# Performance work log

Hardware: AMD Instinct MI355X
Metric: run time of the kernel (lower is better)

Reference implementation:

```python
import jax, jax.numpy as jnp
import numpy as np
from jax import lax

B, S_IN, T_OUT, H, V = 128, 1024, 128, 512, 32


def gru_cell(x, h, Wih, Whh, bih, bhh):
    # PyTorch GRU cell math: gates ordered (r, z, n)
    gi = x @ Wih.T + bih            # (B, 3H)
    gh = h @ Whh.T + bhh            # (B, 3H)
    ir, iz, inn = jnp.split(gi, 3, axis=-1)
    hr, hz, hn = jnp.split(gh, 3, axis=-1)
    r = jax.nn.sigmoid(ir + hr)
    z = jax.nn.sigmoid(iz + hz)
    n = jnp.tanh(inn + r * hn)
    return (1.0 - z) * n + z * h


def setup_inputs() -> dict:
    key = jax.random.key(0)
    ks = jax.random.split(key, 16)
    s = 0.05
    p = lambda k, shape: (jax.random.normal(k, shape, jnp.float32) * s)
    z = lambda n: jnp.zeros((n,), jnp.float32)
    return {
        "x": jax.random.normal(ks[0], (B, S_IN, 2), jnp.float32),
        "embedding": p(ks[1], (V, H)),
        "enc_Wih0": p(ks[2], (3 * H, 2)), "enc_Whh0": p(ks[3], (3 * H, H)),
        "enc_bih0": z(3 * H), "enc_bhh0": z(3 * H),
        "enc_Wih1": p(ks[4], (3 * H, H)), "enc_Whh1": p(ks[5], (3 * H, H)),
        "enc_bih1": z(3 * H), "enc_bhh1": z(3 * H),
        "dec_Wih0": p(ks[6], (3 * H, H)), "dec_Whh0": p(ks[7], (3 * H, H)),
        "dec_bih0": z(3 * H), "dec_bhh0": z(3 * H),
        "dec_Wih1": p(ks[8], (3 * H, H)), "dec_Whh1": p(ks[9], (3 * H, H)),
        "dec_bih1": z(3 * H), "dec_bhh1": z(3 * H),
        "Wq": p(ks[10], (H, H)), "bq": z(H),
        "Wc": p(ks[11], (V, 2 * H)), "bc": z(V),
    }


def reference(x, embedding,
              enc_Wih0, enc_Whh0, enc_bih0, enc_bhh0,
              enc_Wih1, enc_Whh1, enc_bih1, enc_bhh1,
              dec_Wih0, dec_Whh0, dec_bih0, dec_bhh0,
              dec_Wih1, dec_Whh1, dec_bih1, dec_bhh1,
              Wq, bq, Wc, bc):
    b = x.shape[0]
    h_init = jnp.zeros((b, H), x.dtype)

    def run_layer(xs, Wih, Whh, bih, bhh):
        def step(h, xt):
            h2 = gru_cell(xt, h, Wih, Whh, bih, bhh)
            return h2, h2
        return lax.scan(step, h_init, xs)

    # ----- encoder: 2-layer GRU over time -----
    xs = jnp.swapaxes(x, 0, 1)                       # (S, B, 2)
    hT0, ys0 = run_layer(xs, enc_Wih0, enc_Whh0, enc_bih0, enc_bhh0)
    hT1, ys1 = run_layer(ys0, enc_Wih1, enc_Whh1, enc_bih1, enc_bhh1)
    out_enc = jnp.swapaxes(ys1, 0, 1)                # (B, S, H)

    # ----- greedy decoder with Bahdanau-style dot attention -----
    tok0 = jnp.zeros((b,), jnp.int32)                # start token = 0

    def dec_step(carry, _):
        h0, h1, tok = carry
        emb = embedding[tok]                         # (B, H)
        h0n = gru_cell(emb, h0, dec_Wih0, dec_Whh0, dec_bih0, dec_bhh0)
        h1n = gru_cell(h0n, h1, dec_Wih1, dec_Whh1, dec_bih1, dec_bhh1)
        q = h1n @ Wq.T + bq                          # (B, H)
        att = jnp.einsum('bh,bsh->bs', q, out_enc)   # (B, S)
        w = jax.nn.softmax(att, axis=-1)
        ctx = jnp.einsum('bs,bsh->bh', w, out_enc)   # (B, H)
        logits = jnp.concatenate([h1n, ctx], axis=-1) @ Wc.T + bc  # (B, V)
        tok2 = jnp.argmax(logits, axis=-1).astype(jnp.int32)
        return (h0n, h1n, tok2), (logits, w)

    (h0f, h1f, _), (logits_seq, w_seq) = lax.scan(
        dec_step, (hT0, hT1, tok0), None, length=T_OUT)

    vec_out = jnp.swapaxes(logits_seq, 0, 1)         # (B, T_out, V)
    attn_ws = jnp.transpose(w_seq, (1, 2, 0))        # (B, S, T_out)
    hidden = jnp.stack([h0f, h1f], axis=0)           # (n_layers, B, H)
    return vec_out, hidden, attn_ws
```

## Files before the change

### kernel.cpp

```cpp
#include <hip/hip_runtime.h>
#include <hip/hip_fp16.h>
#include <math.h>

#define HH 512
#define BB 128
#define SS 1024
#define TT 128
#define VV 32
#define GG 1536

__device__ __forceinline__ float sigm(float v){ return 1.f/(1.f+expf(-v)); }

struct F8 { float v[8]; };

__device__ __forceinline__ F8 load8(const float* p){
  F8 r;
  float4 a = *reinterpret_cast<const float4*>(p);
  float4 b = *reinterpret_cast<const float4*>(p+4);
  r.v[0]=a.x; r.v[1]=a.y; r.v[2]=a.z; r.v[3]=a.w;
  r.v[4]=b.x; r.v[5]=b.y; r.v[6]=b.z; r.v[7]=b.w;
  return r;
}
__device__ __forceinline__ F8 load8(const __half* p){
  F8 r;
  union { float4 f4; __half2 h2[4]; } u;
  u.f4 = *reinterpret_cast<const float4*>(p);
  #pragma unroll
  for (int i=0;i<4;i++){ float2 f = __half22float2(u.h2[i]); r.v[2*i]=f.x; r.v[2*i+1]=f.y; }
  return r;
}
__device__ __forceinline__ void store_enc(float* p, float v){ *p = v; }
__device__ __forceinline__ void store_enc(__half* p, float v){ *p = __float2half(v); }

__global__ void transpose_k(const float* __restrict__ src, float* __restrict__ dst,
                            int R, int C){
  __shared__ float tile[32][33];
  int c0 = blockIdx.x*32, r0 = blockIdx.y*32;
  int tx = threadIdx.x & 31, ty = threadIdx.x >> 5;
  for (int i = ty; i < 32; i += 8){
    int r = r0 + i, c = c0 + tx;
    tile[i][tx] = (r < R && c < C) ? src[(size_t)r*C + c] : 0.f;
  }
  __syncthreads();
  for (int i = ty; i < 32; i += 8){
    int c = c0 + i, r = r0 + tx;
    if (c < C && r < R) dst[(size_t)c*R + r] = tile[tx][i];
  }
}

template<typename ET>
__global__ __launch_bounds__(192) void enc_step(
    int p,
    const float* __restrict__ x,
    const float* __restrict__ Wih0,
    const float* __restrict__ bih0, const float* __restrict__ bhh0,
    const float* __restrict__ bih1, const float* __restrict__ bhh1,
    const float* __restrict__ Whh0T, const float* __restrict__ Wih1T,
    const float* __restrict__ Whh1T,
    float* __restrict__ gh_all,
    float* __restrict__ h0buf,
    float* __restrict__ h1buf,
    ET* __restrict__ out_enc)
{
  const int bid = blockIdx.x;
  const int xcd = bid & 7, j = bid >> 3;
  const int rc  = xcd*3 + (j % 3);
  const int bch = j / 3;
  const int m   = rc >> 3;
  const int pb  = p & 1;
  if (m == 0 && p >= SS) return;
  if (m >= 1 && p < 1) return;
  const int b0 = bch*8;
  const int tid = threadIdx.x;

  if (m <= 1) {
    float* h0w = h0buf + (size_t)pb*BB*HH;
    for (int idx = tid; idx < 8*HH; idx += 192) {
      int bl = idx >> 9, e = idx & (HH-1);
      int b = b0 + bl;
      float hv;
      if (p == 0) hv = 0.f;
      else {
        int t0 = p - 1;
        float x0v = x[((size_t)b*SS + t0)*2 + 0];
        float x1v = x[((size_t)b*SS + t0)*2 + 1];
        const float* ghp = gh_all + ((size_t)(1-pb)*3 + 0)*BB*GG + (size_t)b*GG;
        float gir = fmaf(x0v, Wih0[e*2],          fmaf(x1v, Wih0[e*2+1],          bih0[e]));
        float giz = fmaf(x0v, Wih0[(HH+e)*2],     fmaf(x1v, Wih0[(HH+e)*2+1],     bih0[HH+e]));
        float gin = fmaf(x0v, Wih0[(2*HH+e)*2],   fmaf(x1v, Wih0[(2*HH+e)*2+1],   bih0[2*HH+e]));
        float ghr = ghp[e]      + bhh0[e];
        float ghz = ghp[HH+e]   + bhh0[HH+e];
        float ghn = ghp[2*HH+e] + bhh0[2*HH+e];
        float hp = (p == 1) ? 0.f : h0buf[(size_t)(1-pb)*BB*HH + (size_t)b*HH + e];
        float r = sigm(gir + ghr);
        float z = sigm(giz + ghz);
        float n = tanhf(fmaf(r, ghn, gin));
        hv = (1.f - z)*n + z*hp;
      }
      h0w[(size_t)b*HH + e] = hv;
    }
  } else {
    float* h1w = h1buf + (size_t)pb*BB*HH;
    for (int idx = tid; idx < 8*HH; idx += 192) {
      int bl = idx >> 9, e = idx & (HH-1);
      int b = b0 + bl;
      float hv;
      if (p <= 1) hv = 0.f;
      else {
        const float* gip = gh_all + ((size_t)(1-pb)*3 + 1)*BB*GG + (size_t)b*GG;
        const float* ghp = gh_all + ((size_t)(1-pb)*3 + 2)*BB*GG + (size_t)b*GG;
        float gir = gip[e]      + bih1[e];
        float giz = gip[HH+e]   + bih1[HH+e];
        float gin = gip[2*HH+e] + bih1[2*HH+e];
        float ghr = ghp[e]      + bhh1[e];
        float ghz = ghp[HH+e]   + bhh1[HH+e];
        float ghn = ghp[2*HH+e] + bhh1[2*HH+e];
        float hp = (p == 2) ? 0.f : h1buf[(size_t)(1-pb)*BB*HH + (size_t)b*HH + e];
        float r = sigm(gir + ghr);
        float z = sigm(giz + ghz);
        float n = tanhf(fmaf(r, ghn, gin));
        hv = (1.f - z)*n + z*hp;
      }
      h1w[(size_t)b*HH + e] = hv;
      if (p >= 2) store_enc(out_enc + ((size_t)b*SS + (p-2))*HH + e, hv);
    }
  }
  __syncthreads();

  const float* WT   = (m == 0) ? Whh0T : (m == 1) ? Wih1T : Whh1T;
  const float* hsrc = (m == 2) ? (h1buf + (size_t)pb*BB*HH) : (h0buf + (size_t)pb*BB*HH);
  const int wv = tid >> 6, lane = tid & 63;
  const int row = (rc & 7)*192 + wv*64 + lane;
  const float* wcol = WT + row;
  float acc[8] = {0,0,0,0,0,0,0,0};
  for (int k = 0; k < HH; k += 4) {
    float w0 = wcol[(size_t)(k+0)*GG];
    float w1 = wcol[(size_t)(k+1)*GG];
    float w2 = wcol[(size_t)(k+2)*GG];
    float w3 = wcol[(size_t)(k+3)*GG];
    #pragma unroll
    for (int i = 0; i < 8; i++) {
      const float4 h4 = *reinterpret_cast<const float4*>(hsrc + (size_t)(b0+i)*HH + k);
      acc[i] = fmaf(w3, h4.w, fmaf(w2, h4.z, fmaf(w1, h4.y, fmaf(w0, h4.x, acc[i]))));
    }
  }
  float* dst = gh_all + ((size_t)pb*3 + m)*BB*GG;
  #pragma unroll
  for (int i = 0; i < 8; i++) dst[(size_t)(b0+i)*GG + row] = acc[i];
}

template<typename ET>
__global__ void enc_bridge(
    const float* __restrict__ gh_all, const float* __restrict__ h1buf,
    const float* __restrict__ bih1, const float* __restrict__ bhh1,
    float* __restrict__ h1init, ET* __restrict__ out_enc)
{
  int idx = blockIdx.x*256 + threadIdx.x;
  int b = idx >> 9, e = idx & (HH-1);
  const float* gip = gh_all + (size_t)1*BB*GG + (size_t)b*GG;
  const float* ghp = gh_all + (size_t)2*BB*GG + (size_t)b*GG;
  float gir = gip[e]      + bih1[e];
  float giz = gip[HH+e]   + bih1[HH+e];
  float gin = gip[2*HH+e] + bih1[2*HH+e];
  float ghr = ghp[e]      + bhh1[e];
  float ghz = ghp[HH+e]   + bhh1[HH+e];
  float ghn = ghp[2*HH+e] + bhh1[2*HH+e];
  float hp = h1buf[(size_t)b*HH + e];
  float r = sigm(gir + ghr);
  float z = sigm(giz + ghz);
  float n = tanhf(fmaf(r, ghn, gin));
  float hv = (1.f - z)*n + z*hp;
  h1init[(size_t)b*HH + e] = hv;
  store_enc(out_enc + ((size_t)b*SS + (SS-1))*HH + e, hv);
}

__global__ __launch_bounds__(192) void dec_step1(
    int t,
    const float* __restrict__ embedding,
    const int* __restrict__ tok,
    const float* __restrict__ bih0d, const float* __restrict__ bhh0d,
    const float* __restrict__ Wih0T, const float* __restrict__ Whh0T,
    const float* __restrict__ h0init,
    float* __restrict__ dgh0,
    float* __restrict__ h0d)
{
  const int bid = blockIdx.x;
  const int xcd = bid & 7, j = bid >> 3;
  const int rc  = xcd*2 + (j & 1);
  const int bch = j >> 1;
  const int m   = rc >> 3;
  const int db  = t & 1;
  const int b0 = bch*8;
  const int tid = threadIdx.x;

  if (m == 1) {
    float* hw = h0d + (size_t)db*BB*HH;
    for (int idx = tid; idx < 8*HH; idx += 192) {
      int bl = idx >> 9, e = idx & (HH-1);
      int b = b0 + bl;
      float hv;
      if (t == 0) hv = h0init[(size_t)b*HH + e];
      else {
        const float* gip = dgh0 + ((size_t)(1-db)*2 + 0)*BB*GG + (size_t)b*GG;
        const float* ghp = dgh0 + ((size_t)(1-db)*2 + 1)*BB*GG + (size_t)b*GG;
        float gir = gip[e]      + bih0d[e];
        float giz = gip[HH+e]   + bih0d[HH+e];
        float gin = gip[2*HH+e] + bih0d[2*HH+e];
        float ghr = ghp[e]      + bhh0d[e];
        float ghz = ghp[HH+e]   + bhh0d[HH+e];
        float ghn = ghp[2*HH+e] + bhh0d[2*HH+e];
        float hp = (t == 1) ? h0init[(size_t)b*HH + e]
                            : h0d[(size_t)(1-db)*BB*HH + (size_t)b*HH + e];
        float r = sigm(gir + ghr);
        float z = sigm(giz + ghz);
        float n = tanhf(fmaf(r, ghn, gin));
        hv = (1.f - z)*n + z*hp;
      }
      hw[(size_t)b*HH + e] = hv;
    }
  }
  __syncthreads();

  const float* WT = (m == 0) ? Wih0T : Whh0T;
  const int wv = tid >> 6, lane = tid & 63;
  const int row = (rc & 7)*192 + wv*64 + lane;
  const float* wcol = WT + row;
  const float* hp8[8];
  #pragma unroll
  for (int i = 0; i < 8; i++)
    hp8[i] = (m == 0) ? (embedding + (size_t)tok[b0+i]*HH)
                      : (h0d + (size_t)db*BB*HH + (size_t)(b0+i)*HH);
  float acc[8] = {0,0,0,0,0,0,0,0};
  for (int k = 0; k < HH; k += 4) {
    float w0 = wcol[(size_t)(k+0)*GG];
    float w1 = wcol[(size_t)(k+1)*GG];
    float w2 = wcol[(size_t)(k+2)*GG];
    float w3 = wcol[(size_t)(k+3)*GG];
    #pragma unroll
    for (int i = 0; i < 8; i++) {
      const float4 h4 = *reinterpret_cast<const float4*>(hp8[i] + k);
      acc[i] = fmaf(w3, h4.w, fmaf(w2, h4.z, fmaf(w1, h4.y, fmaf(w0, h4.x, acc[i]))));
    }
  }
  float* dst = dgh0 + ((size_t)db*2 + m)*BB*GG;
  #pragma unroll
  for (int i = 0; i < 8; i++) dst[(size_t)(b0+i)*GG + row] = acc[i];
}

__global__ __launch_bounds__(192) void dec_step2(
    int t,
    const float* __restrict__ bih0d, const float* __restrict__ bhh0d,
    const float* __restrict__ bih1d, const float* __restrict__ bhh1d,
    const float* __restrict__ Wih1T, const float* __restrict__ Whh1T,
    const float* __restrict__ h1init,
    const float* __restrict__ dgh0,
    const float* __restrict__ h0d,
    float* __restrict__ dgh1,
    float* __restrict__ h1d,
    float* __restrict__ h0n)
{
  const int bid = blockIdx.x;
  const int xcd = bid & 7, j = bid >> 3;
  const int rc  = xcd*2 + (j & 1);
  const int bch = j >> 1;
  const int m   = rc >> 3;
  const int db  = t & 1;
  const int b0 = bch*8;
  const int tid = threadIdx.x;

  if (m == 0) {
    for (int idx = tid; idx < 8*HH; idx += 192) {
      int bl = idx >> 9, e = idx & (HH-1);
      int b = b0 + bl;
      const float* gip = dgh0 + ((size_t)db*2 + 0)*BB*GG + (size_t)b*GG;
      const float* ghp = dgh0 + ((size_t)db*2 + 1)*BB*GG + (size_t)b*GG;
      float gir = gip[e]      + bih0d[e];
      float giz = gip[HH+e]   + bih0d[HH+e];
      float gin = gip[2*HH+e] + bih0d[2*HH+e];
      float ghr = ghp[e]      + bhh0d[e];
      float ghz = ghp[HH+e]   + bhh0d[HH+e];
      float ghn = ghp[2*HH+e] + bhh0d[2*HH+e];
      float hp = h0d[(size_t)db*BB*HH + (size_t)b*HH + e];
      float r = sigm(gir + ghr);
      float z = sigm(giz + ghz);
      float n = tanhf(fmaf(r, ghn, gin));
      h0n[(size_t)b*HH + e] = (1.f - z)*n + z*hp;
    }
  } else {
    float* hw = h1d + (size_t)db*BB*HH;
    for (int idx = tid; idx < 8*HH; idx += 192) {
      int bl = idx >> 9, e = idx & (HH-1);
      int b = b0 + bl;
      float hv;
      if (t == 0) hv = h1init[(size_t)b*HH + e];
      else {
        const float* gip = dgh1 + ((size_t)(1-db)*2 + 0)*BB*GG + (size_t)b*GG;
        const float* ghp = dgh1 + ((size_t)(1-db)*2 + 1)*BB*GG + (size_t)b*GG;
        float gir = gip[e]      + bih1d[e];
        float giz = gip[HH+e]   + bih1d[HH+e];
        float gin = gip[2*HH+e] + bih1d[2*HH+e];
        float ghr = ghp[e]      + bhh1d[e];
        float ghz = ghp[HH+e]   + bhh1d[HH+e];
        float ghn = ghp[2*HH+e] + bhh1d[2*HH+e];
        float hp = (t == 1) ? h1init[(size_t)b*HH + e]
                            : h1d[(size_t)(1-db)*BB*HH + (size_t)b*HH + e];
        float r = sigm(gir + ghr);
        float z = sigm(giz + ghz);
        float n = tanhf(fmaf(r, ghn, gin));
        hv = (1.f - z)*n + z*hp;
      }
      hw[(size_t)b*HH + e] = hv;
    }
  }
  __syncthreads();

  const float* WT = (m == 0) ? Wih1T : Whh1T;
  const float* hsrc = (m == 0) ? h0n : (h1d + (size_t)db*BB*HH);
  const int wv = tid >> 6, lane = tid & 63;
  const int row = (rc & 7)*192 + wv*64 + lane;
  const float* wcol = WT + row;
  float acc[8] = {0,0,0,0,0,0,0,0};
  for (int k = 0; k < HH; k += 4) {
    float w0 = wcol[(size_t)(k+0)*GG];
    float w1 = wcol[(size_t)(k+1)*GG];
    float w2 = wcol[(size_t)(k+2)*GG];
    float w3 = wcol[(size_t)(k+3)*GG];
    #pragma unroll
    for (int i = 0; i < 8; i++) {
      const float4 h4 = *reinterpret_cast<const float4*>(hsrc + (size_t)(b0+i)*HH + k);
      acc[i] = fmaf(w3, h4.w, fmaf(w2, h4.z, fmaf(w1, h4.y, fmaf(w0, h4.x, acc[i]))));
    }
  }
  float* dst = dgh1 + ((size_t)db*2 + m)*BB*GG;
  #pragma unroll
  for (int i = 0; i < 8; i++) dst[(size_t)(b0+i)*GG + row] = acc[i];
}

__global__ __launch_bounds__(256) void dec_step3(
    int t,
    const float* __restrict__ bih1d, const float* __restrict__ bhh1d,
    const float* __restrict__ WqT, const float* __restrict__ bq,
    const float* __restrict__ dgh1, const float* __restrict__ h1d,
    float* __restrict__ h1n, float* __restrict__ qbuf)
{
  const int rc = blockIdx.x & 1, bch = blockIdx.x >> 1;
  const int db = t & 1, b0 = bch*8, tid = threadIdx.x;
  for (int idx = tid; idx < 8*HH; idx += 256) {
    int bl = idx >> 9, e = idx & (HH-1);
    int b = b0 + bl;
    const float* gip = dgh1 + ((size_t)db*2 + 0)*BB*GG + (size_t)b*GG;
    const float* ghp = dgh1 + ((size_t)db*2 + 1)*BB*GG + (size_t)b*GG;
    float gir = gip[e]      + bih1d[e];
    float giz = gip[HH+e]   + bih1d[HH+e];
    float gin = gip[2*HH+e] + bih1d[2*HH+e];
    float ghr = ghp[e]      + bhh1d[e];
    float ghz = ghp[HH+e]   + bhh1d[HH+e];
    float ghn = ghp[2*HH+e] + bhh1d[2*HH+e];
    float hp = h1d[(size_t)db*BB*HH + (size_t)b*HH + e];
    float r = sigm(gir + ghr);
    float z = sigm(giz + ghz);
    float n = tanhf(fmaf(r, ghn, gin));
    h1n[(size_t)b*HH + e] = (1.f - z)*n + z*hp;
  }
  __syncthreads();
  const int wv = tid >> 6, lane = tid & 63;
  const int row = rc*256 + wv*64 + lane;
  const float* wcol = WqT + row;
  float acc[8] = {0,0,0,0,0,0,0,0};
  for (int k = 0; k < HH; k += 4) {
    float w0 = wcol[(size_t)(k+0)*HH];
    float w1 = wcol[(size_t)(k+1)*HH];
    float w2 = wcol[(size_t)(k+2)*HH];
    float w3 = wcol[(size_t)(k+3)*HH];
    #pragma unroll
    for (int i = 0; i < 8; i++) {
      const float4 h4 = *reinterpret_cast<const float4*>(h1n + (size_t)(b0+i)*HH + k);
      acc[i] = fmaf(w3, h4.w, fmaf(w2, h4.z, fmaf(w1, h4.y, fmaf(w0, h4.x, acc[i]))));
    }
  }
  #pragma unroll
  for (int i = 0; i < 8; i++) qbuf[(size_t)(b0+i)*HH + row] = acc[i] + bq[row];
}

template<typename ET>
__global__ __launch_bounds__(256) void dec_attn(
    const float* __restrict__ qbuf, const ET* __restrict__ out_enc,
    float* __restrict__ att, float* __restrict__ pm, float* __restrict__ pl,
    float* __restrict__ pctx)
{
  const int b = blockIdx.x >> 3, sc = blockIdx.x & 7;
  const int tid = threadIdx.x, wv = tid >> 6, lane = tid & 63;
  const F8 q = load8(qbuf + (size_t)b*HH + lane*8);
  const ET* encb = out_enc + (size_t)b*SS*HH;
  float mrun = -1e30f, lrun = 0.f;
  float c[8] = {0,0,0,0,0,0,0,0};
  float attkeep = 0.f;
  const int sbase = sc*128 + wv*32;
  for (int ii = 0; ii < 32; ii++) {
    const F8 e = load8(encb + (size_t)(sbase + ii)*HH + lane*8);
    float d = 0.f;
    #pragma unroll
    for (int j = 0; j < 8; j++) d = fmaf(q.v[j], e.v[j], d);
    #pragma unroll
    for (int off = 32; off >= 1; off >>= 1) d += __shfl_xor(d, off, 64);
    if (lane == ii) attkeep = d;
    float mnew = fmaxf(mrun, d);
    float scal = expf(mrun - mnew);
    float pv = expf(d - mnew);
    lrun = fmaf(lrun, scal, pv);
    #pragma unroll
    for (int j = 0; j < 8; j++) c[j] = fmaf(c[j], scal, pv*e.v[j]);
    mrun = mnew;
  }
  if (lane < 32) att[(size_t)b*SS + sbase + lane] = attkeep;
  __shared__ float lm[4], ll[4];
  __shared__ float lctx[4][HH];
  if (lane == 0) { lm[wv] = mrun; ll[wv] = lrun; }
  #pragma unroll
  for (int j = 0; j < 8; j++) lctx[wv][lane*8+j] = c[j];
  __syncthreads();
  float mb = fmaxf(fmaxf(lm[0],lm[1]), fmaxf(lm[2],lm[3]));
  float e0w = expf(lm[0]-mb), e1w = expf(lm[1]-mb), e2w = expf(lm[2]-mb), e3w = expf(lm[3]-mb);
  if (tid == 0) {
    pm[b*8+sc] = mb;
    pl[b*8+sc] = e0w*ll[0] + e1w*ll[1] + e2w*ll[2] + e3w*ll[3];
  }
  for (int k2 = tid; k2 < HH; k2 += 256) {
    float s = e0w*lctx[0][k2] + e1w*lctx[1][k2] + e2w*lctx[2][k2] + e3w*lctx[3][k2];
    pctx[((size_t)b*8 + sc)*HH + k2] = s;
  }
}

__global__ __launch_bounds__(256) void dec_final(
    int t,
    const float* __restrict__ pm, const float* __restrict__ pl,
    const float* __restrict__ pctx, const float* __restrict__ att,
    const float* __restrict__ h1n,
    const float* __restrict__ WcT, const float* __restrict__ bc,
    float* __restrict__ out_vec, float* __restrict__ out_attn,
    int* __restrict__ tok)
{
  const int b = blockIdx.x, tid = threadIdx.x;
  __shared__ float s_hc[2*HH];
  __shared__ float s_red[8][33];
  float pmv[8], plv[8];
  #pragma unroll
  for (int c = 0; c < 8; c++){ pmv[c] = pm[b*8+c]; plv[c] = pl[b*8+c]; }
  float mg = pmv[0];
  #pragma unroll
  for (int c = 1; c < 8; c++) mg = fmaxf(mg, pmv[c]);
  float epm[8]; float lg = 0.f;
  #pragma unroll
  for (int c = 0; c < 8; c++){ epm[c] = expf(pmv[c]-mg); lg += epm[c]*plv[c]; }
  float inv_lg = 1.f/lg;
  for (int k = tid; k < HH; k += 256) {
    float s = 0.f;
    #pragma unroll
    for (int c = 0; c < 8; c++) s += epm[c]*pctx[((size_t)b*8+c)*HH + k];
    s_hc[HH + k] = s * inv_lg;
    s_hc[k] = h1n[(size_t)b*HH + k];
  }
  __syncthreads();
  for (int s = tid; s < SS; s += 256)
    out_attn[((size_t)b*SS + s)*TT + t] = expf(att[(size_t)b*SS + s] - mg) * inv_lg;
  const int v = tid & 31, part = tid >> 5;
  float pacc = 0.f;
  for (int k = part*128; k < part*128 + 128; k++)
    pacc = fmaf(s_hc[k], WcT[(size_t)k*VV + v], pacc);
  s_red[part][v] = pacc;
  __syncthreads();
  if (tid < 32) {
    float lv = bc[tid];
    #pragma unroll
    for (int c = 0; c < 8; c++) lv += s_red[c][tid];
    out_vec[((size_t)b*TT + t)*VV + tid] = lv;
    float bv = lv; int bi = tid;
    #pragma unroll
    for (int off = 16; off >= 1; off >>= 1) {
      float ov = __shfl_xor(bv, off, 64);
      int   oi = __shfl_xor(bi, off, 64);
      if (ov > bv || (ov == bv && oi < bi)) { bv = ov; bi = oi; }
    }
    if (tid == 0) tok[b] = bi;
  }
}

struct Bufs {
  const float *x, *emb;
  const float *eWih0, *ebih0, *ebhh0, *ebih1, *ebhh1;
  const float *dbih0, *dbhh0, *dbih1, *dbhh1, *bq, *bc;
  float *gh_all, *dgh0, *dgh1;
  float *h0buf, *h1buf, *h0d, *h1d, *h0n, *h1n, *h1init, *qbuf;
  float *att, *pmb, *plb, *pctx;
  int   *tok;
  float *Whh0T, *Wih1T, *Whh1T, *dWih0T, *dWhh0T, *dWih1T, *dWhh1T, *WqT, *WcT;
  float *out_vec, *out_hid, *out_attn;
};

template<typename ET>
static void run_pipeline(const Bufs& B, ET* out_enc, hipStream_t stream) {
  hipMemsetAsync(B.tok, 0, BB*sizeof(int), stream);
  for (int p = 0; p <= SS; p++)
    enc_step<ET><<<dim3(384), dim3(192), 0, stream>>>(p,
        B.x, B.eWih0, B.ebih0, B.ebhh0, B.ebih1, B.ebhh1,
        B.Whh0T, B.Wih1T, B.Whh1T,
        B.gh_all, B.h0buf, B.h1buf, out_enc);
  enc_bridge<ET><<<dim3(256), dim3(256), 0, stream>>>(
      B.gh_all, B.h1buf, B.ebih1, B.ebhh1, B.h1init, out_enc);
  const float* h0init = B.h0buf;

  for (int t = 0; t < TT; t++) {
    dec_step1<<<dim3(256), dim3(192), 0, stream>>>(t,
        B.emb, B.tok, B.dbih0, B.dbhh0, B.dWih0T, B.dWhh0T, h0init, B.dgh0, B.h0d);
    dec_step2<<<dim3(256), dim3(192), 0, stream>>>(t,
        B.dbih0, B.dbhh0, B.dbih1, B.dbhh1, B.dWih1T, B.dWhh1T, B.h1init,
        B.dgh0, B.h0d, B.dgh1, B.h1d, B.h0n);
    dec_step3<<<dim3(32), dim3(256), 0, stream>>>(t,
        B.dbih1, B.dbhh1, B.WqT, B.bq, B.dgh1, B.h1d, B.h1n, B.qbuf);
    dec_attn<ET><<<dim3(1024), dim3(256), 0, stream>>>(
        B.qbuf, out_enc, B.att, B.pmb, B.plb, B.pctx);
    dec_final<<<dim3(128), dim3(256), 0, stream>>>(t,
        B.pmb, B.plb, B.pctx, B.att, B.h1n, B.WcT, B.bc,
        B.out_vec, B.out_attn, B.tok);
  }
  hipMemcpyAsync(B.out_hid, B.h0n, (size_t)BB*HH*sizeof(float),
                 hipMemcpyDeviceToDevice, stream);
  hipMemcpyAsync(B.out_hid + (size_t)BB*HH, B.h1n, (size_t)BB*HH*sizeof(float),
                 hipMemcpyDeviceToDevice, stream);
}

extern "C" void kernel_launch(void* const* d_in, const int* in_sizes, int n_in,
                              void* d_out, int out_size, void* d_ws, size_t ws_size,
                              hipStream_t stream) {
  const float* x      = (const float*)d_in[0];
  const float* emb    = (const float*)d_in[1];
  const float* eWih0  = (const float*)d_in[2];
  const float* eWhh0  = (const float*)d_in[3];
  const float* ebih0  = (const float*)d_in[4];
  const float* ebhh0  = (const float*)d_in[5];
  const float* eWih1  = (const float*)d_in[6];
  const float* eWhh1  = (const float*)d_in[7];
  const float* ebih1  = (const float*)d_in[8];
  const float* ebhh1  = (const float*)d_in[9];
  const float* dWih0  = (const float*)d_in[10];
  const float* dWhh0  = (const float*)d_in[11];
  const float* dbih0  = (const float*)d_in[12];
  const float* dbhh0  = (const float*)d_in[13];
  const float* dWih1  = (const float*)d_in[14];
  const float* dWhh1  = (const float*)d_in[15];
  const float* dbih1  = (const float*)d_in[16];
  const float* dbhh1  = (const float*)d_in[17];
  const float* Wq     = (const float*)d_in[18];
  const float* bq     = (const float*)d_in[19];
  const float* Wc     = (const float*)d_in[20];
  const float* bc     = (const float*)d_in[21];
  (void)in_sizes; (void)n_in; (void)out_size;

  float* ws = (float*)d_ws;
  size_t off = 0;
  auto alloc = [&](size_t n){ float* p = ws + off; off += n; return p; };

  Bufs B;
  B.x = x; B.emb = emb;
  B.eWih0 = eWih0; B.ebih0 = ebih0; B.ebhh0 = ebhh0; B.ebih1 = ebih1; B.ebhh1 = ebhh1;
  B.dbih0 = dbih0; B.dbhh0 = dbhh0; B.dbih1 = dbih1; B.dbhh1 = dbhh1;
  B.bq = bq; B.bc = bc;

  B.gh_all  = alloc((size_t)2*3*BB*GG);
  B.dgh0    = alloc((size_t)2*2*BB*GG);
  B.dgh1    = alloc((size_t)2*2*BB*GG);
  B.h0buf   = alloc((size_t)2*BB*HH);
  B.h1buf   = alloc((size_t)2*BB*HH);
  B.h0d     = alloc((size_t)2*BB*HH);
  B.h1d     = alloc((size_t)2*BB*HH);
  B.h0n     = alloc((size_t)BB*HH);
  B.h1n     = alloc((size_t)BB*HH);
  B.h1init  = alloc((size_t)BB*HH);
  B.qbuf    = alloc((size_t)BB*HH);
  B.att     = alloc((size_t)BB*SS);
  B.pmb     = alloc((size_t)BB*8);
  B.plb     = alloc((size_t)BB*8);
  B.pctx    = alloc((size_t)BB*8*HH);
  B.tok     = (int*)alloc((size_t)BB);
  B.Whh0T   = alloc((size_t)HH*GG);
  B.Wih1T   = alloc((size_t)HH*GG);
  B.Whh1T   = alloc((size_t)HH*GG);
  B.dWih0T  = alloc((size_t)HH*GG);
  B.dWhh0T  = alloc((size_t)HH*GG);
  B.dWih1T  = alloc((size_t)HH*GG);
  B.dWhh1T  = alloc((size_t)HH*GG);
  B.WqT     = alloc((size_t)HH*HH);
  B.WcT     = alloc((size_t)2*HH*VV);

  B.out_vec  = (float*)d_out;
  B.out_hid  = (float*)d_out + (size_t)BB*TT*VV;
  B.out_attn = (float*)d_out + (size_t)BB*TT*VV + (size_t)2*BB*HH;

  dim3 tb(256);
  transpose_k<<<dim3(16,48), tb, 0, stream>>>(eWhh0, B.Whh0T, GG, HH);
  transpose_k<<<dim3(16,48), tb, 0, stream>>>(eWih1, B.Wih1T, GG, HH);
  transpose_k<<<dim3(16,48), tb, 0, stream>>>(eWhh1, B.Whh1T, GG, HH);
  transpose_k<<<dim3(16,48), tb, 0, stream>>>(dWih0, B.dWih0T, GG, HH);
  transpose_k<<<dim3(16,48), tb, 0, stream>>>(dWhh0, B.dWhh0T, GG, HH);
  transpose_k<<<dim3(16,48), tb, 0, stream>>>(dWih1, B.dWih1T, GG, HH);
  transpose_k<<<dim3(16,48), tb, 0, stream>>>(dWhh1, B.dWhh1T, GG, HH);
  transpose_k<<<dim3(16,16), tb, 0, stream>>>(Wq, B.WqT, HH, HH);
  transpose_k<<<dim3(32,1),  tb, 0, stream>>>(Wc, B.WcT, VV, 2*HH);

  const size_t enc_elems = (size_t)BB*SS*HH;
  const size_t need32 = (off + enc_elems) * sizeof(float);
  if (ws_size >= need32) {
    float* out_enc = ws + off;
    run_pipeline<float>(B, out_enc, stream);
  } else {
    __half* out_enc = reinterpret_cast<__half*>(ws + off);
    run_pipeline<__half>(B, out_enc, stream);
  }
}
```

Measured before the change: 95.91 ms.

## Pack weights into float4 k-chunks and stage hidden states in shared memory

Replaces the transposed weight layout with a packed layout where each row's four consecutive k values sit in one float4, so every thread issues one 16-byte load per four k steps. The next chunk is prefetched one iteration ahead. The GEMV inputs (hidden states or embeddings) are written to LDS during the gate phase and read from there instead of from global memory. tanhf is also replaced by an exp-based fast_tanh. The cost is 16KB of LDS per block, which may limit occupancy, plus a small precision difference in tanh.

```diff
diff --git a/kernel.cpp b/kernel.cpp
--- a/kernel.cpp
+++ b/kernel.cpp
@@ -10,6 +10,12 @@
 #define GG 1536
 
 __device__ __forceinline__ float sigm(float v){ return 1.f/(1.f+expf(-v)); }
+__device__ __forceinline__ float fast_tanh(float x){
+  float ax = fabsf(x);
+  float t = expf(-2.f*ax);
+  float r = (1.f - t)/(1.f + t);
+  return copysignf(r, x);
+}
 
 struct F8 { float v[8]; };
 
@@ -48,6 +54,26 @@
   }
 }
 
+__global__ void pack_w(const float* __restrict__ src, float* __restrict__ dst, int R){
+  int idx = blockIdx.x*256 + threadIdx.x;
+  int r = idx >> 9, k = idx & 511;
+  dst[((size_t)(k>>2)*R + r)*4 + (k&3)] = src[idx];
+}
+
+__device__ __forceinline__ void dot8(const float4* __restrict__ wp, int row, int NR,
+                                     const float4* sh4, float acc[8]){
+  float4 wc = wp[row];
+  for (int kc = 0; kc < 128; kc++) {
+    float4 wn = wp[(size_t)(kc+1)*NR + row];
+    #pragma unroll
+    for (int i = 0; i < 8; i++) {
+      float4 h4 = sh4[i*128 + kc];
+      acc[i] = fmaf(wc.w, h4.w, fmaf(wc.z, h4.z, fmaf(wc.y, h4.y, fmaf(wc.x, h4.x, acc[i]))));
+    }
+    wc = wn;
+  }
+}
+
 template<typename ET>
 __global__ __launch_bounds__(192) void enc_step(
     int p,
@@ -55,13 +81,15 @@
     const float* __restrict__ Wih0,
     const float* __restrict__ bih0, const float* __restrict__ bhh0,
     const float* __restrict__ bih1, const float* __restrict__ bhh1,
-    const float* __restrict__ Whh0T, const float* __restrict__ Wih1T,
-    const float* __restrict__ Whh1T,
+    const float* __restrict__ Whh0P, const float* __restrict__ Wih1P,
+    const float* __restrict__ Whh1P,
     float* __restrict__ gh_all,
     float* __restrict__ h0buf,
     float* __restrict__ h1buf,
     ET* __restrict__ out_enc)
 {
+  __shared__ float4 sh4[8*128];
+  float* shs = (float*)sh4;
   const int bid = blockIdx.x;
   const int xcd = bid & 7, j = bid >> 3;
   const int rc  = xcd*3 + (j % 3);
@@ -94,10 +122,11 @@
         float hp = (p == 1) ? 0.f : h0buf[(size_t)(1-pb)*BB*HH + (size_t)b*HH + e];
         float r = sigm(gir + ghr);
         float z = sigm(giz + ghz);
-        float n = tanhf(fmaf(r, ghn, gin));
+        float n = fast_tanh(fmaf(r, ghn, gin));
         hv = (1.f - z)*n + z*hp;
       }
       h0w[(size_t)b*HH + e] = hv;
+      shs[idx] = hv;
     }
   } else {
     float* h1w = h1buf + (size_t)pb*BB*HH;
@@ -118,32 +147,21 @@
         float hp = (p == 2) ? 0.f : h1buf[(size_t)(1-pb)*BB*HH + (size_t)b*HH + e];
         float r = sigm(gir + ghr);
         float z = sigm(giz + ghz);
-        float n = tanhf(fmaf(r, ghn, gin));
+        float n = fast_tanh(fmaf(r, ghn, gin));
         hv = (1.f - z)*n + z*hp;
       }
       h1w[(size_t)b*HH + e] = hv;
+      shs[idx] = hv;
       if (p >= 2) store_enc(out_enc + ((size_t)b*SS + (p-2))*HH + e, hv);
     }
   }
   __syncthreads();
 
-  const float* WT   = (m == 0) ? Whh0T : (m == 1) ? Wih1T : Whh1T;
-  const float* hsrc = (m == 2) ? (h1buf + (size_t)pb*BB*HH) : (h0buf + (size_t)pb*BB*HH);
+  const float4* WP = (const float4*)((m == 0) ? Whh0P : (m == 1) ? Wih1P : Whh1P);
   const int wv = tid >> 6, lane = tid & 63;
   const int row = (rc & 7)*192 + wv*64 + lane;
-  const float* wcol = WT + row;
   float acc[8] = {0,0,0,0,0,0,0,0};
-  for (int k = 0; k < HH; k += 4) {
-    float w0 = wcol[(size_t)(k+0)*GG];
-    float w1 = wcol[(size_t)(k+1)*GG];
-    float w2 = wcol[(size_t)(k+2)*GG];
-    float w3 = wcol[(size_t)(k+3)*GG];
-    #pragma unroll
-    for (int i = 0; i < 8; i++) {
-      const float4 h4 = *reinterpret_cast<const float4*>(hsrc + (size_t)(b0+i)*HH + k);
-      acc[i] = fmaf(w3, h4.w, fmaf(w2, h4.z, fmaf(w1, h4.y, fmaf(w0, h4.x, acc[i]))));
-    }
-  }
+  dot8(WP, row, GG, sh4, acc);
   float* dst = gh_all + ((size_t)pb*3 + m)*BB*GG;
   #pragma unroll
   for (int i = 0; i < 8; i++) dst[(size_t)(b0+i)*GG + row] = acc[i];
@@ -168,7 +186,7 @@
   float hp = h1buf[(size_t)b*HH + e];
   float r = sigm(gir + ghr);
   float z = sigm(giz + ghz);
-  float n = tanhf(fmaf(r, ghn, gin));
+  float n = fast_tanh(fmaf(r, ghn, gin));
   float hv = (1.f - z)*n + z*hp;
   h1init[(size_t)b*HH + e] = hv;
   store_enc(out_enc + ((size_t)b*SS + (SS-1))*HH + e, hv);
@@ -179,11 +197,13 @@
     const float* __restrict__ embedding,
     const int* __restrict__ tok,
     const float* __restrict__ bih0d, const float* __restrict__ bhh0d,
-    const float* __restrict__ Wih0T, const float* __restrict__ Whh0T,
+    const float* __restrict__ Wih0P, const float* __restrict__ Whh0P,
     const float* __restrict__ h0init,
     float* __restrict__ dgh0,
     float* __restrict__ h0d)
 {
+  __shared__ float4 sh4[8*128];
+  float* shs = (float*)sh4;
   const int bid = blockIdx.x;
   const int xcd = bid & 7, j = bid >> 3;
   const int rc  = xcd*2 + (j & 1);
@@ -213,35 +233,26 @@
                             : h0d[(size_t)(1-db)*BB*HH + (size_t)b*HH + e];
         float r = sigm(gir + ghr);
         float z = sigm(giz + ghz);
-        float n = tanhf(fmaf(r, ghn, gin));
+        float n = fast_tanh(fmaf(r, ghn, gin));
         hv = (1.f - z)*n + z*hp;
       }
       hw[(size_t)b*HH + e] = hv;
-    }
-  }
-  __syncthreads();
-
-  const float* WT = (m == 0) ? Wih0T : Whh0T;
+      shs[idx] = hv;
+    }
+  } else {
+    for (int idx = tid; idx < 8*HH; idx += 192) {
+      int bl = idx >> 9, e = idx & (HH-1);
+      int tk = tok[b0 + bl];
+      shs[idx] = embedding[(size_t)tk*HH + e];
+    }
+  }
+  __syncthreads();
+
+  const float4* WP = (const float4*)((m == 0) ? Wih0P : Whh0P);
   const int wv = tid >> 6, lane = tid & 63;
   const int row = (rc & 7)*192 + wv*64 + lane;
-  const float* wcol = WT + row;
-  const float* hp8[8];
-  #pragma unroll
-  for (int i = 0; i < 8; i++)
-    hp8[i] = (m == 0) ? (embedding + (size_t)tok[b0+i]*HH)
-                      : (h0d + (size_t)db*BB*HH + (size_t)(b0+i)*HH);
   float acc[8] = {0,0,0,0,0,0,0,0};
-  for (int k = 0; k < HH; k += 4) {
-    float w0 = wcol[(size_t)(k+0)*GG];
-    float w1 = wcol[(size_t)(k+1)*GG];
-    float w2 = wcol[(size_t)(k+2)*GG];
-    float w3 = wcol[(size_t)(k+3)*GG];
-    #pragma unroll
-    for (int i = 0; i < 8; i++) {
-      const float4 h4 = *reinterpret_cast<const float4*>(hp8[i] + k);
-      acc[i] = fmaf(w3, h4.w, fmaf(w2, h4.z, fmaf(w1, h4.y, fmaf(w0, h4.x, acc[i]))));
-    }
-  }
+  dot8(WP, row, GG, sh4, acc);
   float* dst = dgh0 + ((size_t)db*2 + m)*BB*GG;
   #pragma unroll
   for (int i = 0; i < 8; i++) dst[(size_t)(b0+i)*GG + row] = acc[i];
@@ -251,7 +262,7 @@
     int t,
     const float* __restrict__ bih0d, const float* __restrict__ bhh0d,
     const float* __restrict__ bih1d, const float* __restrict__ bhh1d,
-    const float* __restrict__ Wih1T, const float* __restrict__ Whh1T,
+    const float* __restrict__ Wih1P, const float* __restrict__ Whh1P,
     const float* __restrict__ h1init,
     const float* __restrict__ dgh0,
     const float* __restrict__ h0d,
@@ -259,6 +270,8 @@
     float* __restrict__ h1d,
     float* __restrict__ h0n)
 {
+  __shared__ float4 sh4[8*128];
+  float* shs = (float*)sh4;
   const int bid = blockIdx.x;
   const int xcd = bid & 7, j = bid >> 3;
   const int rc  = xcd*2 + (j & 1);
@@ -283,8 +296,10 @@
       float hp = h0d[(size_t)db*BB*HH + (size_t)b*HH + e];
       float r = sigm(gir + ghr);
       float z = sigm(giz + ghz);
-      float n = tanhf(fmaf(r, ghn, gin));
-      h0n[(size_t)b*HH + e] = (1.f - z)*n + z*hp;
+      float n = fast_tanh(fmaf(r, ghn, gin));
+      float hv = (1.f - z)*n + z*hp;
+      h0n[(size_t)b*HH + e] = hv;
+      shs[idx] = hv;
     }
   } else {
     float* hw = h1d + (size_t)db*BB*HH;
@@ -306,31 +321,20 @@
                             : h1d[(size_t)(1-db)*BB*HH + (size_t)b*HH + e];
         float r = sigm(gir + ghr);
         float z = sigm(giz + ghz);
-        float n = tanhf(fmaf(r, ghn, gin));
+        float n = fast_tanh(fmaf(r, ghn, gin));
         hv = (1.f - z)*n + z*hp;
       }
       hw[(size_t)b*HH + e] = hv;
-    }
-  }
-  __syncthreads();
-
-  const float* WT = (m == 0) ? Wih1T : Whh1T;
-  const float* hsrc = (m == 0) ? h0n : (h1d + (size_t)db*BB*HH);
+      shs[idx] = hv;
+    }
+  }
+  __syncthreads();
+
+  const float4* WP = (const float4*)((m == 0) ? Wih1P : Whh1P);
   const int wv = tid >> 6, lane = tid & 63;
   const int row = (rc & 7)*192 + wv*64 + lane;
-  const float* wcol = WT + row;
   float acc[8] = {0,0,0,0,0,0,0,0};
-  for (int k = 0; k < HH; k += 4) {
-    float w0 = wcol[(size_t)(k+0)*GG];
-    float w1 = wcol[(size_t)(k+1)*GG];
-    float w2 = wcol[(size_t)(k+2)*GG];
-    float w3 = wcol[(size_t)(k+3)*GG];
-    #pragma unroll
-    for (int i = 0; i < 8; i++) {
-      const float4 h4 = *reinterpret_cast<const float4*>(hsrc + (size_t)(b0+i)*HH + k);
-      acc[i] = fmaf(w3, h4.w, fmaf(w2, h4.z, fmaf(w1, h4.y, fmaf(w0, h4.x, acc[i]))));
-    }
-  }
+  dot8(WP, row, GG, sh4, acc);
   float* dst = dgh1 + ((size_t)db*2 + m)*BB*GG;
   #pragma unroll
   for (int i = 0; i < 8; i++) dst[(size_t)(b0+i)*GG + row] = acc[i];
@@ -339,10 +343,12 @@
 __global__ __launch_bounds__(256) void dec_step3(
     int t,
     const float* __restrict__ bih1d, const float* __restrict__ bhh1d,
-    const float* __restrict__ WqT, const float* __restrict__ bq,
+    const float* __restrict__ WqP, const float* __restrict__ bq,
     const float* __restrict__ dgh1, const float* __restrict__ h1d,
     float* __restrict__ h1n, float* __restrict__ qbuf)
 {
+  __shared__ float4 sh4[8*128];
+  float* shs = (float*)sh4;
   const int rc = blockIdx.x & 1, bch = blockIdx.x >> 1;
   const int db = t & 1, b0 = bch*8, tid = threadIdx.x;
   for (int idx = tid; idx < 8*HH; idx += 256) {
@@ -359,25 +365,16 @@
     float hp = h1d[(size_t)db*BB*HH + (size_t)b*HH + e];
     float r = sigm(gir + ghr);
     float z = sigm(giz + ghz);
-    float n = tanhf(fmaf(r, ghn, gin));
-    h1n[(size_t)b*HH + e] = (1.f - z)*n + z*hp;
+    float n = fast_tanh(fmaf(r, ghn, gin));
+    float hv = (1.f - z)*n + z*hp;
+    h1n[(size_t)b*HH + e] = hv;
+    shs[idx] = hv;
   }
   __syncthreads();
   const int wv = tid >> 6, lane = tid & 63;
   const int row = rc*256 + wv*64 + lane;
-  const float* wcol = WqT + row;
   float acc[8] = {0,0,0,0,0,0,0,0};
-  for (int k = 0; k < HH; k += 4) {
-    float w0 = wcol[(size_t)(k+0)*HH];
-    float w1 = wcol[(size_t)(k+1)*HH];
-    float w2 = wcol[(size_t)(k+2)*HH];
-    float w3 = wcol[(size_t)(k+3)*HH];
-    #pragma unroll
-    for (int i = 0; i < 8; i++) {
-      const float4 h4 = *reinterpret_cast<const float4*>(h1n + (size_t)(b0+i)*HH + k);
-      acc[i] = fmaf(w3, h4.w, fmaf(w2, h4.z, fmaf(w1, h4.y, fmaf(w0, h4.x, acc[i]))));
-    }
-  }
+  dot8((const float4*)WqP, row, HH, sh4, acc);
   #pragma unroll
   for (int i = 0; i < 8; i++) qbuf[(size_t)(b0+i)*HH + row] = acc[i] + bq[row];
 }
@@ -493,7 +490,7 @@
   float *h0buf, *h1buf, *h0d, *h1d, *h0n, *h1n, *h1init, *qbuf;
   float *att, *pmb, *plb, *pctx;
   int   *tok;
-  float *Whh0T, *Wih1T, *Whh1T, *dWih0T, *dWhh0T, *dWih1T, *dWhh1T, *WqT, *WcT;
+  float *Whh0P, *Wih1P, *Whh1P, *dWih0P, *dWhh0P, *dWih1P, *dWhh1P, *WqP, *WcT;
   float *out_vec, *out_hid, *out_attn;
 };
 
@@ -503,7 +500,7 @@
   for (int p = 0; p <= SS; p++)
     enc_step<ET><<<dim3(384), dim3(192), 0, stream>>>(p,
         B.x, B.eWih0, B.ebih0, B.ebhh0, B.ebih1, B.ebhh1,
-        B.Whh0T, B.Wih1T, B.Whh1T,
+        B.Whh0P, B.Wih1P, B.Whh1P,
         B.gh_all, B.h0buf, B.h1buf, out_enc);
   enc_bridge<ET><<<dim3(256), dim3(256), 0, stream>>>(
       B.gh_all, B.h1buf, B.ebih1, B.ebhh1, B.h1init, out_enc);
@@ -511,12 +508,12 @@
 
   for (int t = 0; t < TT; t++) {
     dec_step1<<<dim3(256), dim3(192), 0, stream>>>(t,
-        B.emb, B.tok, B.dbih0, B.dbhh0, B.dWih0T, B.dWhh0T, h0init, B.dgh0, B.h0d);
+        B.emb, B.tok, B.dbih0, B.dbhh0, B.dWih0P, B.dWhh0P, h0init, B.dgh0, B.h0d);
     dec_step2<<<dim3(256), dim3(192), 0, stream>>>(t,
-        B.dbih0, B.dbhh0, B.dbih1, B.dbhh1, B.dWih1T, B.dWhh1T, B.h1init,
+        B.dbih0, B.dbhh0, B.dbih1, B.dbhh1, B.dWih1P, B.dWhh1P, B.h1init,
         B.dgh0, B.h0d, B.dgh1, B.h1d, B.h0n);
     dec_step3<<<dim3(32), dim3(256), 0, stream>>>(t,
-        B.dbih1, B.dbhh1, B.WqT, B.bq, B.dgh1, B.h1d, B.h1n, B.qbuf);
+        B.dbih1, B.dbhh1, B.WqP, B.bq, B.dgh1, B.h1d, B.h1n, B.qbuf);
     dec_attn<ET><<<dim3(1024), dim3(256), 0, stream>>>(
         B.qbuf, out_enc, B.att, B.pmb, B.plb, B.pctx);
     dec_final<<<dim3(128), dim3(256), 0, stream>>>(t,
@@ -559,6 +556,8 @@
   float* ws = (float*)d_ws;
   size_t off = 0;
   auto alloc = [&](size_t n){ float* p = ws + off; off += n; return p; };
+  const size_t PKB = (size_t)GG*HH + 4*GG;
+  const size_t PKQ = (size_t)HH*HH + 4*HH;
 
   Bufs B;
   B.x = x; B.emb = emb;
@@ -582,14 +581,14 @@
   B.plb     = alloc((size_t)BB*8);
   B.pctx    = alloc((size_t)BB*8*HH);
   B.tok     = (int*)alloc((size_t)BB);
-  B.Whh0T   = alloc((size_t)HH*GG);
-  B.Wih1T   = alloc((size_t)HH*GG);
-  B.Whh1T   = alloc((size_t)HH*GG);
-  B.dWih0T  = alloc((size_t)HH*GG);
-  B.dWhh0T  = alloc((size_t)HH*GG);
-  B.dWih1T  = alloc((size_t)HH*GG);
-  B.dWhh1T  = alloc((size_t)HH*GG);
-  B.WqT     = alloc((size_t)HH*HH);
+  B.Whh0P   = alloc(PKB);
+  B.Wih1P   = alloc(PKB);
+  B.Whh1P   = alloc(PKB);
+  B.dWih0P  = alloc(PKB);
+  B.dWhh0P  = alloc(PKB);
+  B.dWih1P  = alloc(PKB);
+  B.dWhh1P  = alloc(PKB);
+  B.WqP     = alloc(PKQ);
   B.WcT     = alloc((size_t)2*HH*VV);
 
   B.out_vec  = (float*)d_out;
@@ -597,14 +596,14 @@
   B.out_attn = (float*)d_out + (size_t)BB*TT*VV + (size_t)2*BB*HH;
 
   dim3 tb(256);
-  transpose_k<<<dim3(16,48), tb, 0, stream>>>(eWhh0, B.Whh0T, GG, HH);
-  transpose_k<<<dim3(16,48), tb, 0, stream>>>(eWih1, B.Wih1T, GG, HH);
-  transpose_k<<<dim3(16,48), tb, 0, stream>>>(eWhh1, B.Whh1T, GG, HH);
-  transpose_k<<<dim3(16,48), tb, 0, stream>>>(dWih0, B.dWih0T, GG, HH);
-  transpose_k<<<dim3(16,48), tb, 0, stream>>>(dWhh0, B.dWhh0T, GG, HH);
-  transpose_k<<<dim3(16,48), tb, 0, stream>>>(dWih1, B.dWih1T, GG, HH);
-  transpose_k<<<dim3(16,48), tb, 0, stream>>>(dWhh1, B.dWhh1T, GG, HH);
-  transpose_k<<<dim3(16,16), tb, 0, stream>>>(Wq, B.WqT, HH, HH);
+  pack_w<<<dim3(GG*HH/256), tb, 0, stream>>>(eWhh0, B.Whh0P, GG);
+  pack_w<<<dim3(GG*HH/256), tb, 0, stream>>>(eWih1, B.Wih1P, GG);
+  pack_w<<<dim3(GG*HH/256), tb, 0, stream>>>(eWhh1, B.Whh1P, GG);
+  pack_w<<<dim3(GG*HH/256), tb, 0, stream>>>(dWih0, B.dWih0P, GG);
+  pack_w<<<dim3(GG*HH/256), tb, 0, stream>>>(dWhh0, B.dWhh0P, GG);
+  pack_w<<<dim3(GG*HH/256), tb, 0, stream>>>(dWih1, B.dWih1P, GG);
+  pack_w<<<dim3(GG*HH/256), tb, 0, stream>>>(dWhh1, B.dWhh1P, GG);
+  pack_w<<<dim3(HH*HH/256), tb, 0, stream>>>(Wq, B.WqP, HH);
   transpose_k<<<dim3(32,1),  tb, 0, stream>>>(Wc, B.WcT, VV, 2*HH);
 
   const size_t enc_elems = (size_t)BB*SS*HH;
```

New measurement: 97.19 ms. Within noise of the previous version (+1.3%).
